# Performance work log

Hardware: AMD Instinct MI355X
Metric: run time of the kernel (lower is better)

The kernel has to match this reference:

```python
import jax, jax.numpy as jnp
import numpy as np

B, TV, TL = 4, 13600, 256
VD, LD, E, H = 256, 768, 256, 8
HD = E // H
SCALE = HD ** -0.5
CLAMP = 50000.0
NEG = -9e15


def _xavier(k, out_d, in_d):
    lim = np.sqrt(6.0 / (in_d + out_d)).astype(np.float32)
    return jax.random.uniform(k, (out_d, in_d), minval=-lim, maxval=lim, dtype=jnp.float32)


def setup_inputs() -> dict:
    key = jax.random.key(0)
    ks = jax.random.split(key, 10)
    return {
        "v": jax.random.normal(ks[0], (B, TV, VD), dtype=jnp.float32),
        "l": jax.random.normal(ks[1], (B, TL, LD), dtype=jnp.float32),
        "v_pos": jax.random.normal(ks[2], (B, TV, VD), dtype=jnp.float32),
        "attention_mask_v": jnp.ones((B, TV), dtype=jnp.float32),
        "attention_mask_l": jnp.ones((B, TL), dtype=jnp.float32),
        "Wq": _xavier(ks[3], E, VD), "bq": jnp.zeros((E,), jnp.float32),
        "Wk": _xavier(ks[4], E, LD), "bk": jnp.zeros((E,), jnp.float32),
        "Wvv": _xavier(ks[5], E, VD), "bvv": jnp.zeros((E,), jnp.float32),
        "Wvl": _xavier(ks[6], E, LD), "bvl": jnp.zeros((E,), jnp.float32),
        "Wov": _xavier(ks[7], VD, E), "bov": jnp.zeros((VD,), jnp.float32),
        "Wol": _xavier(ks[8], LD, E), "bol": jnp.zeros((LD,), jnp.float32),
    }


def _heads(x):  # [B, T, E] -> [B, H, T, HD]
    b, t, _ = x.shape
    return x.reshape(b, t, H, HD).transpose(0, 2, 1, 3)


def reference(v, l, v_pos, attention_mask_v, attention_mask_l,
              Wq, bq, Wk, bk, Wvv, bvv, Wvl, bvl, Wov, bov, Wol, bol):
    # projections (eval mode: dropout disabled)
    q = _heads(((v + v_pos) @ Wq.T + bq) * SCALE)        # [B,H,TV,HD]
    k = _heads(l @ Wk.T + bk)                             # [B,H,TL,HD]
    val_v = _heads(v @ Wvv.T + bvv)                       # [B,H,TV,HD]
    val_l = _heads(l @ Wvl.T + bvl)                       # [B,H,TL,HD]

    # shared scores, computed once: [B,H,TV,TL]
    aw = jnp.einsum('bhtd,bhsd->bhts', q, k)
    aw = jnp.clip(aw, -CLAMP, CLAMP)

    # language-direction scores: transpose, stabilize, clamp
    aw_l = aw.transpose(0, 1, 3, 2)                       # [B,H,TL,TV]
    aw_l = aw_l - jnp.max(aw_l, axis=-1, keepdims=True)
    aw_l = jnp.clip(aw_l, -CLAMP, CLAMP)
    # torch masked_fill(mask==0, NEG) then + : nonzero mask values are ADDED
    mv = jnp.where(attention_mask_v == 0, NEG, attention_mask_v)[:, None, None, :]
    aw_l = aw_l + mv
    p_l = jax.nn.softmax(aw_l, axis=-1)

    # vision-direction scores
    ml = jnp.where(attention_mask_l == 0, NEG, attention_mask_l)[:, None, None, :]
    p_v = jax.nn.softmax(aw + ml, axis=-1)

    out_v = jnp.einsum('bhts,bhsd->bhtd', p_v, val_l)     # [B,H,TV,HD]
    out_l = jnp.einsum('bhst,bhtd->bhsd', p_l, val_v)     # [B,H,TL,HD]
    out_v = out_v.transpose(0, 2, 1, 3).reshape(B, TV, E) @ Wov.T + bov
    out_l = out_l.transpose(0, 2, 1, 3).reshape(B, TL, E) @ Wol.T + bol
    return (out_v, out_l)
```

## Files before the change

### kernel.cpp

```cpp
#include <hip/hip_runtime.h>
#include <math.h>


typedef unsigned short u16;
typedef unsigned int   u32;
typedef __attribute__((ext_vector_type(2))) u32 u32x2;
typedef __attribute__((ext_vector_type(4))) u16 us4;
typedef __attribute__((ext_vector_type(8))) u16 us8;
typedef __attribute__((ext_vector_type(8))) short s8b;
typedef __attribute__((ext_vector_type(4))) float f4;

#define B_   4
#define TV_  13600
#define TL_  256
#define VD_  256
#define LD_  768
#define E_   256
#define H_   8
#define HD_  32
#define NREC (B_*H_*TL_)

static constexpr float SCALE_  = 0.17677669529663687f;
static constexpr float NEG_    = -9e15f;
static constexpr float LOG2E_  = 1.4426950408889634f;

__device__ __forceinline__ float bf2f(u16 x) {
    return __uint_as_float(((u32)x) << 16);
}
__device__ __forceinline__ u16 f2bf(float f) {
    u32 u = __float_as_uint(f);
    u += 0x7fffu + ((u >> 16) & 1u);
    return (u16)(u >> 16);
}
__device__ __forceinline__ u32 cvtpk(float lo, float hi) {
    u32 r;
    asm("v_cvt_pk_bf16_f32 %0, %1, %2" : "=v"(r) : "v"(lo), "v"(hi));
    return r;
}
__device__ __forceinline__ float bflo(u32 w) { return __uint_as_float(w << 16); }
__device__ __forceinline__ float bfhi(u32 w) { return __uint_as_float(w & 0xffff0000u); }

__device__ __forceinline__ s8b frag32(const u16* base, int row, int q) {
    int slot = q ^ ((row >> 1) & 3);
    return *(const s8b*)(base + row * 32 + slot * 8);
}

__global__ void sniff_kernel(const void* __restrict__ mask, int* __restrict__ flag) {
    if (threadIdx.x == 0 && blockIdx.x == 0) {
        u32 w = *(const u32*)mask;
        *flag = (w == 0x3F800000u) ? 1 : 0;
    }
}

__global__ __launch_bounds__(256) void prep_v_kernel(
    const int* __restrict__ flag, const void* __restrict__ v,
    const void* __restrict__ vp, u16* __restrict__ vb, u16* __restrict__ vqb)
{
    const bool f32 = (*flag != 0);
    const size_t n = (size_t)B_ * TV_ * VD_;
    size_t i = ((size_t)blockIdx.x * 256 + threadIdx.x) * 4;
    const size_t stride = (size_t)gridDim.x * 256 * 4;
    for (; i < n; i += stride) {
        float a[4], b[4];
        if (f32) {
            float4 x = ((const float4*)v)[i >> 2];
            float4 y = ((const float4*)vp)[i >> 2];
            a[0]=x.x; a[1]=x.y; a[2]=x.z; a[3]=x.w;
            b[0]=y.x; b[1]=y.y; b[2]=y.z; b[3]=y.w;
        } else {
            us4 x = ((const us4*)v)[i >> 2];
            us4 y = ((const us4*)vp)[i >> 2];
            #pragma unroll
            for (int j = 0; j < 4; ++j) { a[j]=bf2f(x[j]); b[j]=bf2f(y[j]); }
        }
        us4 o1, o2;
        #pragma unroll
        for (int j = 0; j < 4; ++j) { o1[j]=f2bf(a[j]); o2[j]=f2bf(a[j]+b[j]); }
        ((us4*)vb)[i >> 2] = o1;
        ((us4*)vqb)[i >> 2] = o2;
    }
}

struct Seg { const void* src; void* dst; int n; int toF32; };
struct PrepArgs { Seg s[13]; };

__global__ __launch_bounds__(256) void prep_rest_kernel(
    const int* __restrict__ flag, PrepArgs args)
{
    const bool f32 = (*flag != 0);
    for (int k = 0; k < 13; ++k) {
        Seg sg = args.s[k];
        for (int j = blockIdx.x * 256 + threadIdx.x; j < sg.n;
             j += gridDim.x * 256) {
            float x = f32 ? ((const float*)sg.src)[j] : bf2f(((const u16*)sg.src)[j]);
            if (sg.toF32) ((float*)sg.dst)[j] = x;
            else          ((u16*)sg.dst)[j]   = f2bf(x);
        }
    }
}

template<int OMODE, int TDIM>
__global__ __launch_bounds__(256) void gemm_mfma(
    const int* __restrict__ flag,
    const u16* __restrict__ A, const u16* __restrict__ W,
    const float* __restrict__ bias, void* __restrict__ C, size_t c_off,
    int N, int K, float scale)
{
    __shared__ __align__(16) u16 As[128 * 32];
    __shared__ __align__(16) u16 Bs[128 * 32];
    const int tid  = threadIdx.x;
    const int lane = tid & 63, wid = tid >> 6;
    const int wm = wid >> 1, wn = wid & 1;
    const size_t m0 = (size_t)blockIdx.x * 128;
    const int n0 = blockIdx.y * 128;

    const int srow = tid >> 1;
    const int half = tid & 1;
    const int ssw  = (srow >> 1) & 3;
    const int sl0  = half * 2, sl1 = half * 2 + 1;

    f4 acc[4][4];
    #pragma unroll
    for (int i = 0; i < 4; ++i)
        #pragma unroll
        for (int j = 0; j < 4; ++j) acc[i][j] = (f4){0.f, 0.f, 0.f, 0.f};

    for (int k0 = 0; k0 < K; k0 += 32) {
        {
            const u16* ga = A + (m0 + srow) * (size_t)K + k0;
            *(us8*)&As[srow*32 + sl0*8] = *(const us8*)(ga + (sl0 ^ ssw) * 8);
            *(us8*)&As[srow*32 + sl1*8] = *(const us8*)(ga + (sl1 ^ ssw) * 8);
            const u16* gb = W + ((size_t)(n0 + srow)) * (size_t)K + k0;
            *(us8*)&Bs[srow*32 + sl0*8] = *(const us8*)(gb + (sl0 ^ ssw) * 8);
            *(us8*)&Bs[srow*32 + sl1*8] = *(const us8*)(gb + (sl1 ^ ssw) * 8);
        }
        __syncthreads();
        s8b af[4], bf[4];
        const int q = lane >> 4;
        #pragma unroll
        for (int mt = 0; mt < 4; ++mt)
            af[mt] = frag32(As, wm*64 + mt*16 + (lane & 15), q);
        #pragma unroll
        for (int nt = 0; nt < 4; ++nt)
            bf[nt] = frag32(Bs, wn*64 + nt*16 + (lane & 15), q);
        __builtin_amdgcn_s_setprio(1);
        #pragma unroll
        for (int mt = 0; mt < 4; ++mt)
            #pragma unroll
            for (int nt = 0; nt < 4; ++nt)
                acc[mt][nt] = __builtin_amdgcn_mfma_f32_16x16x32_bf16(
                    af[mt], bf[nt], acc[mt][nt], 0, 0, 0);
        __builtin_amdgcn_s_setprio(0);
        __syncthreads();
    }

    const int q = lane >> 4;
    const bool f32out = (OMODE == 1) ? (*flag != 0) : false;
    #pragma unroll
    for (int nt = 0; nt < 4; ++nt) {
        const int col = n0 + wn*64 + nt*16 + (lane & 15);
        const float bv = bias[col];
        #pragma unroll
        for (int mt = 0; mt < 4; ++mt) {
            #pragma unroll
            for (int reg = 0; reg < 4; ++reg) {
                const int row = (int)m0 + wm*64 + mt*16 + q*4 + reg;
                const float val = (acc[mt][nt][reg] + bv) * scale;
                if (OMODE == 2) {
                    const int b = row / TDIM, t = row - b * TDIM;
                    ((u16*)C)[(((size_t)(b*H_ + (col >> 5)))*TDIM + t)*HD_ + (col & 31)]
                        = f2bf(val);
                } else {
                    const size_t idx = c_off + (size_t)row * N + col;
                    if (f32out) ((float*)C)[idx] = val;
                    else        ((u16*)C)[idx]   = f2bf(val);
                }
            }
        }
    }
}

__global__ __launch_bounds__(256, 4) void attn_v_mfma(
    const int* __restrict__ flag,
    const u16* __restrict__ qm, const u16* __restrict__ km,
    const u16* __restrict__ vm, const void* __restrict__ maskl,
    u16* __restrict__ outm)
{
    __shared__ __align__(16) u16 Qs[64 * 32];
    __shared__ __align__(16) u16 Ks[256 * 32];
    __shared__ __align__(16) u16 VTs[32 * 264];
    __shared__ float mls[256];

    const int tid = threadIdx.x, lane = tid & 63, wid = tid >> 6;
    const int bb = blockIdx.z, hh = blockIdx.y;
    const int bh = bb*H_ + hh;
    const int t0 = blockIdx.x * 64;
    const int q  = lane >> 4;
    const int l15 = lane & 15;

    {
        int row = tid >> 2, slot = tid & 3;
        int sw = (row >> 1) & 3;
        int tg = t0 + row; if (tg >= TV_) tg = TV_ - 1;
        const u16* gp = qm + ((size_t)(bh*TV_ + tg)) * HD_;
        *(us8*)&Qs[row*32 + slot*8] = *(const us8*)(gp + ((slot ^ sw) * 8));
    }
    {
        int s = tid, sw = (s >> 1) & 3;
        const u16* gp = km + ((size_t)(bh*TL_ + s)) * HD_;
        #pragma unroll
        for (int slot = 0; slot < 4; ++slot)
            *(us8*)&Ks[s*32 + slot*8] = *(const us8*)(gp + ((slot ^ sw) * 8));
    }
    {
        int s = tid;
        const u16* gp = vm + ((size_t)(bh*TL_ + s)) * HD_;
        #pragma unroll
        for (int d0 = 0; d0 < 32; d0 += 8) {
            us8 vv = *(const us8*)(gp + d0);
            #pragma unroll
            for (int j = 0; j < 8; ++j) VTs[(d0 + j)*264 + s] = vv[j];
        }
        float mv = (*flag) ? ((const float*)maskl)[(size_t)bb*TL_ + s]
                           : bf2f(((const u16*)maskl)[(size_t)bb*TL_ + s]);
        mls[s] = (mv == 0.0f) ? NEG_ : mv;
    }
    __syncthreads();

    const s8b qf = frag32(Qs, wid*16 + l15, q);
    f4 sacc[16];
    __builtin_amdgcn_s_setprio(1);
    #pragma unroll
    for (int mt = 0; mt < 16; ++mt) {
        s8b kf = frag32(Ks, mt*16 + l15, q);
        f4 z = {0.f, 0.f, 0.f, 0.f};
        sacc[mt] = __builtin_amdgcn_mfma_f32_16x16x32_bf16(kf, qf, z, 0, 0, 0);
    }
    __builtin_amdgcn_s_setprio(0);

    float vmax = -1e30f;
    #pragma unroll
    for (int mt = 0; mt < 16; ++mt) {
        f4 mv4 = *(const f4*)&mls[mt*16 + q*4];
        #pragma unroll
        for (int r = 0; r < 4; ++r) {
            float v = sacc[mt][r] + mv4[r];
            sacc[mt][r] = v;
            vmax = fmaxf(vmax, v);
        }
    }
    vmax = fmaxf(vmax, __shfl_xor(vmax, 16));
    vmax = fmaxf(vmax, __shfl_xor(vmax, 32));

    const float nmL = -vmax * LOG2E_;
    float sum = 0.f;
    u32 pw[32];
    #pragma unroll
    for (int mt = 0; mt < 16; ++mt) {
        float p0 = exp2f(fmaf(sacc[mt][0], LOG2E_, nmL));
        float p1 = exp2f(fmaf(sacc[mt][1], LOG2E_, nmL));
        float p2 = exp2f(fmaf(sacc[mt][2], LOG2E_, nmL));
        float p3 = exp2f(fmaf(sacc[mt][3], LOG2E_, nmL));
        u32 w0 = cvtpk(p0, p1), w1 = cvtpk(p2, p3);
        pw[2*mt]   = w0;
        pw[2*mt+1] = w1;
        sum += bflo(w0) + bfhi(w0) + bflo(w1) + bfhi(w1);
    }
    sum += __shfl_xor(sum, 16);
    sum += __shfl_xor(sum, 32);
    float Lreg[4];
    #pragma unroll
    for (int r = 0; r < 4; ++r) Lreg[r] = __shfl(sum, q*4 + r);

    __syncthreads();

    u16* myP = Ks + wid * (16 * 40);
    f4 oacc[2];
    oacc[0] = (f4){0.f,0.f,0.f,0.f};
    oacc[1] = (f4){0.f,0.f,0.f,0.f};
    __builtin_amdgcn_s_setprio(1);
    #pragma unroll
    for (int ks = 0; ks < 8; ++ks) {
        *(u32x2*)&myP[l15*40 + q*4]      = (u32x2){pw[4*ks],   pw[4*ks+1]};
        *(u32x2*)&myP[l15*40 + 16 + q*4] = (u32x2){pw[4*ks+2], pw[4*ks+3]};
        s8b pa = *(const s8b*)&myP[l15*40 + q*8];
        #pragma unroll
        for (int nt = 0; nt < 2; ++nt) {
            s8b vb = *(const s8b*)&VTs[(nt*16 + l15)*264 + ks*32 + q*8];
            oacc[nt] = __builtin_amdgcn_mfma_f32_16x16x32_bf16(pa, vb, oacc[nt], 0, 0, 0);
        }
    }
    __builtin_amdgcn_s_setprio(0);

    #pragma unroll
    for (int r = 0; r < 4; ++r) {
        const int tg = t0 + wid*16 + q*4 + r;
        if (tg < TV_) {
            const float inv = 1.0f / Lreg[r];
            #pragma unroll
            for (int nt = 0; nt < 2; ++nt)
                outm[((size_t)(bb*TV_ + tg)) * E_ + hh*HD_ + nt*16 + l15] =
                    f2bf(oacc[nt][r] * inv);
        }
    }
}

__global__ __launch_bounds__(256, 4) void attn_l_mfma(
    const int* __restrict__ flag,
    const u16* __restrict__ qm, const u16* __restrict__ km,
    const u16* __restrict__ vm, const void* __restrict__ maskv,
    u16* __restrict__ part_o, float2* __restrict__ part_ml,
    int nchunk, int chunk)
{
    __shared__ __align__(16) u16 smem0[256 * 40];
    __shared__ __align__(16) u16 Qs[32 * 32];
    __shared__ __align__(16) u16 VTs[32 * 32];
    __shared__ float mvs[32];

    const int tid = threadIdx.x, lane = tid & 63, wid = tid >> 6;
    const int bb = blockIdx.z, hh = blockIdx.y, tc = blockIdx.x;
    const int bh = bb*H_ + hh;
    const int q = lane >> 4, l15 = lane & 15;
    const bool f32m = (*flag != 0);

    {
        int s = tid, sw = (s >> 1) & 3;
        const u16* gp = km + ((size_t)(bh*TL_ + s)) * HD_;
        #pragma unroll
        for (int slot = 0; slot < 4; ++slot)
            *(us8*)&smem0[s*32 + slot*8] = *(const us8*)(gp + ((slot ^ sw) * 8));
    }
    s8b bk[4];
    #pragma unroll
    for (int st = 0; st < 4; ++st)
        bk[st] = frag32(smem0, wid*64 + st*16 + l15, q);

    float m_s[4], l_s[4];
    f4 oacc[2][4];
    #pragma unroll
    for (int st = 0; st < 4; ++st) {
        m_s[st] = -1e30f; l_s[st] = 0.f;
        oacc[0][st] = (f4){0.f,0.f,0.f,0.f};
        oacc[1][st] = (f4){0.f,0.f,0.f,0.f};
    }

    const int nstep = chunk >> 5;
    for (int step = 0; step < nstep; ++step) {
        const int t0 = tc * chunk + step * 32;
        if (tid < 128) {
            int row = tid >> 2, slot = tid & 3;
            int sw = (row >> 1) & 3;
            const u16* gp = qm + ((size_t)(bh*TV_ + t0 + row)) * HD_;
            *(us8*)&Qs[row*32 + slot*8] = *(const us8*)(gp + ((slot ^ sw) * 8));
        } else {
            int t2 = tid - 128;
            int trow = t2 >> 2, d0 = (t2 & 3) * 8;
            us8 vv = *(const us8*)(vm + ((size_t)(bh*TV_ + t0 + trow)) * HD_ + d0);
            #pragma unroll
            for (int j = 0; j < 8; ++j) {
                int d = d0 + j;
                VTs[d*32 + (((trow >> 3) ^ ((d >> 1) & 3)) * 8) + (trow & 7)] = vv[j];
            }
        }
        if (tid < 32) {
            float mv = f32m ? ((const float*)maskv)[(size_t)bb*TV_ + t0 + tid]
                            : bf2f(((const u16*)maskv)[(size_t)bb*TV_ + t0 + tid]);
            mvs[tid] = (mv == 0.0f) ? NEG_ : mv;
        }
        __syncthreads();

        s8b aq0 = frag32(Qs, l15, q);
        s8b aq1 = frag32(Qs, 16 + l15, q);
        f4 sacc[2][4];
        __builtin_amdgcn_s_setprio(1);
        #pragma unroll
        for (int st = 0; st < 4; ++st) {
            f4 zz = {0.f, 0.f, 0.f, 0.f};
            sacc[0][st] = __builtin_amdgcn_mfma_f32_16x16x32_bf16(aq0, bk[st], zz, 0, 0, 0);
            sacc[1][st] = __builtin_amdgcn_mfma_f32_16x16x32_bf16(aq1, bk[st], zz, 0, 0, 0);
        }
        __builtin_amdgcn_s_setprio(0);

        float mvq[2][4];
        #pragma unroll
        for (int tt = 0; tt < 2; ++tt)
            #pragma unroll
            for (int r = 0; r < 4; ++r) mvq[tt][r] = mvs[tt*16 + q*4 + r];

        #pragma unroll
        for (int st = 0; st < 4; ++st) {
            float v[2][4];
            float vmax = -1e30f;
            #pragma unroll
            for (int tt = 0; tt < 2; ++tt)
                #pragma unroll
                for (int r = 0; r < 4; ++r) {
                    v[tt][r] = sacc[tt][st][r] + mvq[tt][r];
                    vmax = fmaxf(vmax, v[tt][r]);
                }
            vmax = fmaxf(vmax, __shfl_xor(vmax, 16));
            vmax = fmaxf(vmax, __shfl_xor(vmax, 32));
            float m = m_s[st];
            if (__any(vmax > m + 8.0f)) {
                float nm = fmaxf(m, vmax);
                float al = exp2f((m - nm) * LOG2E_);
                l_s[st] *= al;
                #pragma unroll
                for (int dt = 0; dt < 2; ++dt)
                    #pragma unroll
                    for (int r = 0; r < 4; ++r) oacc[dt][st][r] *= al;
                m_s[st] = m = nm;
            }
            const float nmL = -m * LOG2E_;
            const int ls = wid*64 + st*16 + l15;
            float ps = 0.f;
            #pragma unroll
            for (int tt = 0; tt < 2; ++tt) {
                float p0 = exp2f(fmaf(v[tt][0], LOG2E_, nmL));
                float p1 = exp2f(fmaf(v[tt][1], LOG2E_, nmL));
                float p2 = exp2f(fmaf(v[tt][2], LOG2E_, nmL));
                float p3 = exp2f(fmaf(v[tt][3], LOG2E_, nmL));
                u32 w0 = cvtpk(p0, p1), w1 = cvtpk(p2, p3);
                *(u32x2*)&smem0[ls*40 + tt*16 + q*4] = (u32x2){w0, w1};
                ps += bflo(w0) + bfhi(w0) + bflo(w1) + bfhi(w1);
            }
            ps += __shfl_xor(ps, 16);
            ps += __shfl_xor(ps, 32);
            l_s[st] += ps;
        }

        s8b av0 = frag32(VTs, l15, q);
        s8b av1 = frag32(VTs, 16 + l15, q);
        __builtin_amdgcn_s_setprio(1);
        #pragma unroll
        for (int st = 0; st < 4; ++st) {
            s8b bp = *(const s8b*)&smem0[(wid*64 + st*16 + l15)*40 + q*8];
            oacc[0][st] = __builtin_amdgcn_mfma_f32_16x16x32_bf16(av0, bp, oacc[0][st], 0, 0, 0);
            oacc[1][st] = __builtin_amdgcn_mfma_f32_16x16x32_bf16(av1, bp, oacc[1][st], 0, 0, 0);
        }
        __builtin_amdgcn_s_setprio(0);
        __syncthreads();
    }

    #pragma unroll
    for (int st = 0; st < 4; ++st) {
        const int s = wid*64 + st*16 + l15;
        const size_t R = (size_t)bh*TL_ + s;
        u16* ro = part_o + ((size_t)tc*NREC + R)*32;
        u32 w0 = cvtpk(oacc[0][st][0], oacc[0][st][1]);
        u32 w1 = cvtpk(oacc[0][st][2], oacc[0][st][3]);
        u32 w2 = cvtpk(oacc[1][st][0], oacc[1][st][1]);
        u32 w3 = cvtpk(oacc[1][st][2], oacc[1][st][3]);
        *(u32x2*)&ro[q*4]      = (u32x2){w0, w1};
        *(u32x2*)&ro[16 + q*4] = (u32x2){w2, w3};
        if (q == 0) {
            float2 mlv; mlv.x = m_s[st]; mlv.y = l_s[st];
            part_ml[(size_t)tc*NREC + R] = mlv;
        }
    }
}

__global__ __launch_bounds__(256) void attn_l_merge(
    const u16* __restrict__ part_o, const float2* __restrict__ part_ml,
    u16* __restrict__ outm, int nchunk)
{
    const int R = blockIdx.x * 8 + (threadIdx.x >> 5);
    const int d = threadIdx.x & 31;
    float m = -1e30f;
    for (int c = 0; c < nchunk; ++c)
        m = fmaxf(m, part_ml[(size_t)c*NREC + R].x);
    float L = 0.f, o = 0.f;
    for (int c = 0; c < nchunk; ++c) {
        float2 mlv = part_ml[(size_t)c*NREC + R];
        float w = exp2f((mlv.x - m) * LOG2E_);
        L += mlv.y * w;
        o += bf2f(part_o[((size_t)c*NREC + R)*32 + d]) * w;
    }
    o /= L;
    const int bb = R >> 11, hh = (R >> 8) & 7, ss = R & 255;
    outm[(size_t)(bb*TL_ + ss) * E_ + hh*HD_ + d] = f2bf(o);
}

extern "C" void kernel_launch(void* const* d_in, const int* in_sizes, int n_in,
                              void* d_out, int out_size, void* d_ws, size_t ws_size,
                              hipStream_t stream)
{
    const void* v     = d_in[0];
    const void* l     = d_in[1];
    const void* vpos  = d_in[2];
    const void* maskv = d_in[3];
    const void* maskl = d_in[4];
    const void* Wq  = d_in[5];   const void* bq  = d_in[6];
    const void* Wk  = d_in[7];   const void* bk  = d_in[8];
    const void* Wvv = d_in[9];   const void* bvv = d_in[10];
    const void* Wvl = d_in[11];  const void* bvl = d_in[12];
    const void* Wov = d_in[13];  const void* bov = d_in[14];
    const void* Wol = d_in[15];  const void* bol = d_in[16];

    const size_t BIG   = (size_t)B_*TV_*E_*2;
    const size_t TLBUF = (size_t)B_*TL_*E_*2;
    const size_t LBUF  = (size_t)B_*TL_*LD_*2;
    auto part_bytes = [](int nc) { return (size_t)NREC * (size_t)nc * 72; };

    const size_t fixed = 512 + 2*(BIG+256) + (LBUF+256) + 3*(TLBUF+256)
                       + (131072+256)*3 + (393216+256)*3 + (8192+256);
    const int cand[3] = {25, 17, 5};
    int nchunk = 5;
    for (int i = 0; i < 3; ++i)
        if (fixed + part_bytes(cand[i]) + 512 <= ws_size) { nchunk = cand[i]; break; }
    const int chunk = TV_ / nchunk;

    char* ws = (char*)d_ws;
    size_t off = 0;
    auto carve = [&](size_t bytes) -> char* {
        char* p = ws + off;
        off += (bytes + 255) & ~(size_t)255;
        return p;
    };
    int*   flag    = (int*)carve(512);
    u16*   slot1   = (u16*)carve(BIG);
    u16*   slot2   = (u16*)carve(BIG);
    u16*   lb      = (u16*)carve(LBUF);
    u16*   k_ws    = (u16*)carve(TLBUF);
    u16*   vall_ws = (u16*)carve(TLBUF);
    u16*   attnl_ws= (u16*)carve(TLBUF);
    u16*   wqb     = (u16*)carve(131072);
    u16*   wkb     = (u16*)carve(393216);
    u16*   wvvb    = (u16*)carve(131072);
    u16*   wvlb    = (u16*)carve(393216);
    u16*   wovb    = (u16*)carve(131072);
    u16*   wolb    = (u16*)carve(393216);
    float* biasf   = (float*)carve(8192);
    u16*    part_o  = (u16*)carve((size_t)nchunk*NREC*64);
    float2* part_ml = (float2*)carve((size_t)nchunk*NREC*8);

    u16* vb    = slot1;
    u16* vqb   = slot2;
    u16* valv  = slot2;
    u16* attnv = slot1;
    u16* q_ws  = (u16*)d_out;

    float* bqf  = biasf;        float* bkf  = biasf + 256;
    float* bvvf = biasf + 512;  float* bvlf = biasf + 768;
    float* bovf = biasf + 1024; float* bolf = biasf + 1280;

    const dim3 blk(256);
    const size_t outl_off = (size_t)B_*TV_*VD_;

    sniff_kernel<<<1, 64, 0, stream>>>(maskv, flag);

    prep_v_kernel<<<2048, blk, 0, stream>>>(flag, v, vpos, vb, vqb);
    PrepArgs pa;
    pa.s[0]  = { l,   lb,   B_*TL_*LD_, 0 };
    pa.s[1]  = { Wq,  wqb,  E_*VD_,     0 };
    pa.s[2]  = { Wk,  wkb,  E_*LD_,     0 };
    pa.s[3]  = { Wvv, wvvb, E_*VD_,     0 };
    pa.s[4]  = { Wvl, wvlb, E_*LD_,     0 };
    pa.s[5]  = { Wov, wovb, VD_*E_,     0 };
    pa.s[6]  = { Wol, wolb, LD_*E_,     0 };
    pa.s[7]  = { bq,  bqf,  E_,  1 };
    pa.s[8]  = { bk,  bkf,  E_,  1 };
    pa.s[9]  = { bvv, bvvf, E_,  1 };
    pa.s[10] = { bvl, bvlf, E_,  1 };
    pa.s[11] = { bov, bovf, VD_, 1 };
    pa.s[12] = { bol, bolf, LD_, 1 };
    prep_rest_kernel<<<256, blk, 0, stream>>>(flag, pa);

    gemm_mfma<2, TV_><<<dim3(425, 2), blk, 0, stream>>>(flag, vqb, wqb,  bqf,  q_ws,    0, E_, VD_, SCALE_);
    gemm_mfma<2, TV_><<<dim3(425, 2), blk, 0, stream>>>(flag, vb,  wvvb, bvvf, valv,    0, E_, VD_, 1.0f);
    gemm_mfma<2, TL_><<<dim3(8,   2), blk, 0, stream>>>(flag, lb,  wkb,  bkf,  k_ws,    0, E_, LD_, 1.0f);
    gemm_mfma<2, TL_><<<dim3(8,   2), blk, 0, stream>>>(flag, lb,  wvlb, bvlf, vall_ws, 0, E_, LD_, 1.0f);

    attn_l_mfma <<<dim3(nchunk, H_, B_), blk, 0, stream>>>(flag, q_ws, k_ws, valv, maskv, part_o, part_ml, nchunk, chunk);
    attn_l_merge<<<dim3(B_*H_*TL_/8),    blk, 0, stream>>>(part_o, part_ml, attnl_ws, nchunk);
    attn_v_mfma <<<dim3((TV_+63)/64, H_, B_), blk, 0, stream>>>(flag, q_ws, k_ws, vall_ws, maskl, attnv);

    gemm_mfma<1, 1><<<dim3(425, 2), blk, 0, stream>>>(flag, attnv,    wovb, bovf, d_out, 0,        VD_, E_, 1.0f);
    gemm_mfma<1, 1><<<dim3(8,   6), blk, 0, stream>>>(flag, attnl_ws, wolb, bolf, d_out, outl_off, LD_, E_, 1.0f);
}
```

Before: 454.7 us.

## Split language-direction attention blocks across two halves of TL rows

```diff
diff --git a/kernel.cpp b/kernel.cpp
--- a/kernel.cpp
+++ b/kernel.cpp
@@ -305,44 +305,42 @@
     }
 }
 
-__global__ __launch_bounds__(256, 4) void attn_l_mfma(
+__global__ __launch_bounds__(256, 8) void attn_l_mfma(
     const int* __restrict__ flag,
     const u16* __restrict__ qm, const u16* __restrict__ km,
     const u16* __restrict__ vm, const void* __restrict__ maskv,
     u16* __restrict__ part_o, float2* __restrict__ part_ml,
     int nchunk, int chunk)
 {
-    __shared__ __align__(16) u16 smem0[256 * 40];
+    __shared__ __align__(16) u16 smem0[128 * 40];
     __shared__ __align__(16) u16 Qs[32 * 32];
     __shared__ __align__(16) u16 VTs[32 * 32];
     __shared__ float mvs[32];
 
     const int tid = threadIdx.x, lane = tid & 63, wid = tid >> 6;
-    const int bb = blockIdx.z, hh = blockIdx.y, tc = blockIdx.x;
+    const int bb = blockIdx.z, hh = blockIdx.y;
+    const int tc  = blockIdx.x >> 1;
+    const int s0b = (blockIdx.x & 1) * 128;
     const int bh = bb*H_ + hh;
     const int q = lane >> 4, l15 = lane & 15;
     const bool f32m = (*flag != 0);
 
     {
-        int s = tid, sw = (s >> 1) & 3;
-        const u16* gp = km + ((size_t)(bh*TL_ + s)) * HD_;
-        #pragma unroll
-        for (int slot = 0; slot < 4; ++slot)
-            *(us8*)&smem0[s*32 + slot*8] = *(const us8*)(gp + ((slot ^ sw) * 8));
-    }
-    s8b bk[4];
-    #pragma unroll
-    for (int st = 0; st < 4; ++st)
-        bk[st] = frag32(smem0, wid*64 + st*16 + l15, q);
-
-    float m_s[4], l_s[4];
-    f4 oacc[2][4];
-    #pragma unroll
-    for (int st = 0; st < 4; ++st) {
-        m_s[st] = -1e30f; l_s[st] = 0.f;
-        oacc[0][st] = (f4){0.f,0.f,0.f,0.f};
-        oacc[1][st] = (f4){0.f,0.f,0.f,0.f};
-    }
+        int row = tid >> 1, half = tid & 1;
+        int sw = (row >> 1) & 3;
+        const u16* gp = km + ((size_t)(bh*TL_ + s0b + row)) * HD_;
+        int sl0 = half*2, sl1 = half*2 + 1;
+        *(us8*)&smem0[row*32 + sl0*8] = *(const us8*)(gp + ((sl0 ^ sw) * 8));
+        *(us8*)&smem0[row*32 + sl1*8] = *(const us8*)(gp + ((sl1 ^ sw) * 8));
+    }
+    s8b bk0 = frag32(smem0, wid*32 + l15, q);
+    s8b bk1 = frag32(smem0, wid*32 + 16 + l15, q);
+
+    float m_s[2], l_s[2];
+    f4 oacc[2][2];
+    m_s[0] = m_s[1] = -1e30f;
+    l_s[0] = l_s[1] = 0.f;
+    oacc[0][0] = oacc[0][1] = oacc[1][0] = oacc[1][1] = (f4){0.f,0.f,0.f,0.f};
 
     const int nstep = chunk >> 5;
     for (int step = 0; step < nstep; ++step) {
@@ -371,13 +369,14 @@
 
         s8b aq0 = frag32(Qs, l15, q);
         s8b aq1 = frag32(Qs, 16 + l15, q);
-        f4 sacc[2][4];
+        f4 sacc[2][2];
         __builtin_amdgcn_s_setprio(1);
-        #pragma unroll
-        for (int st = 0; st < 4; ++st) {
+        {
             f4 zz = {0.f, 0.f, 0.f, 0.f};
-            sacc[0][st] = __builtin_amdgcn_mfma_f32_16x16x32_bf16(aq0, bk[st], zz, 0, 0, 0);
-            sacc[1][st] = __builtin_amdgcn_mfma_f32_16x16x32_bf16(aq1, bk[st], zz, 0, 0, 0);
+            sacc[0][0] = __builtin_amdgcn_mfma_f32_16x16x32_bf16(aq0, bk0, zz, 0, 0, 0);
+            sacc[0][1] = __builtin_amdgcn_mfma_f32_16x16x32_bf16(aq0, bk1, zz, 0, 0, 0);
+            sacc[1][0] = __builtin_amdgcn_mfma_f32_16x16x32_bf16(aq1, bk0, zz, 0, 0, 0);
+            sacc[1][1] = __builtin_amdgcn_mfma_f32_16x16x32_bf16(aq1, bk1, zz, 0, 0, 0);
         }
         __builtin_amdgcn_s_setprio(0);
 
@@ -388,7 +387,7 @@
             for (int r = 0; r < 4; ++r) mvq[tt][r] = mvs[tt*16 + q*4 + r];
 
         #pragma unroll
-        for (int st = 0; st < 4; ++st) {
+        for (int st = 0; st < 2; ++st) {
             float v[2][4];
             float vmax = -1e30f;
             #pragma unroll
@@ -412,7 +411,7 @@
                 m_s[st] = m = nm;
             }
             const float nmL = -m * LOG2E_;
-            const int ls = wid*64 + st*16 + l15;
+            const int ls = wid*32 + st*16 + l15;
             float ps = 0.f;
             #pragma unroll
             for (int tt = 0; tt < 2; ++tt) {
@@ -433,8 +432,8 @@
         s8b av1 = frag32(VTs, 16 + l15, q);
         __builtin_amdgcn_s_setprio(1);
         #pragma unroll
-        for (int st = 0; st < 4; ++st) {
-            s8b bp = *(const s8b*)&smem0[(wid*64 + st*16 + l15)*40 + q*8];
+        for (int st = 0; st < 2; ++st) {
+            s8b bp = *(const s8b*)&smem0[(wid*32 + st*16 + l15)*40 + q*8];
             oacc[0][st] = __builtin_amdgcn_mfma_f32_16x16x32_bf16(av0, bp, oacc[0][st], 0, 0, 0);
             oacc[1][st] = __builtin_amdgcn_mfma_f32_16x16x32_bf16(av1, bp, oacc[1][st], 0, 0, 0);
         }
@@ -443,8 +442,8 @@
     }
 
     #pragma unroll
-    for (int st = 0; st < 4; ++st) {
-        const int s = wid*64 + st*16 + l15;
+    for (int st = 0; st < 2; ++st) {
+        const int s = s0b + wid*32 + st*16 + l15;
         const size_t R = (size_t)bh*TL_ + s;
         u16* ro = part_o + ((size_t)tc*NREC + R)*32;
         u32 w0 = cvtpk(oacc[0][st][0], oacc[0][st][1]);
@@ -571,8 +570,8 @@
     gemm_mfma<2, TL_><<<dim3(8,   2), blk, 0, stream>>>(flag, lb,  wkb,  bkf,  k_ws,    0, E_, LD_, 1.0f);
     gemm_mfma<2, TL_><<<dim3(8,   2), blk, 0, stream>>>(flag, lb,  wvlb, bvlf, vall_ws, 0, E_, LD_, 1.0f);
 
-    attn_l_mfma <<<dim3(nchunk, H_, B_), blk, 0, stream>>>(flag, q_ws, k_ws, valv, maskv, part_o, part_ml, nchunk, chunk);
-    attn_l_merge<<<dim3(B_*H_*TL_/8),    blk, 0, stream>>>(part_o, part_ml, attnl_ws, nchunk);
+    attn_l_mfma <<<dim3(nchunk*2, H_, B_), blk, 0, stream>>>(flag, q_ws, k_ws, valv, maskv, part_o, part_ml, nchunk, chunk);
+    attn_l_merge<<<dim3(B_*H_*TL_/8),      blk, 0, stream>>>(part_o, part_ml, attnl_ws, nchunk);
     attn_v_mfma <<<dim3((TV_+63)/64, H_, B_), blk, 0, stream>>>(flag, q_ws, k_ws, vall_ws, maskl, attnv);
 
     gemm_mfma<1, 1><<<dim3(425, 2), blk, 0, stream>>>(flag, attnv,    wovb, bovf, d_out, 0,        VD_, E_, 1.0f);
```

Measured after the change: 471.4 us. +3.7%, slower.
